# Kernel optimization log

Measured on AMD Instinct MI355X. Metric: run time of the kernel, lower is better.

## Reference

```python
import jax, jax.numpy as jnp
import numpy as np

DIM = 1024
HEADS = 16
DIM_HEAD = 64
NUM_KV_HEADS = 4
INNER = HEADS * DIM_HEAD          # 1024
KV_DIM = NUM_KV_HEADS * DIM_HEAD  # 256
SCALE = DIM_HEAD ** -0.5


def setup_inputs() -> dict:
    key = jax.random.key(0)
    ks = jax.random.split(key, 7)
    B, S = 2, 2048
    x = jax.random.normal(ks[0], (B, S, DIM), dtype=jnp.float32)
    init = lambda k, shape: jax.random.normal(k, shape, dtype=jnp.float32) * (shape[0] ** -0.5)
    return {
        "x": x,
        "ln_gamma": jnp.ones((DIM,), jnp.float32),
        "ln_beta": jnp.zeros((DIM,), jnp.float32),
        "w_q": init(ks[1], (DIM, INNER)),
        "w_k": init(ks[2], (DIM, KV_DIM)),
        "w_v": init(ks[3], (DIM, KV_DIM)),
        "w_o": init(ks[4], (INNER, DIM)),
        "b_o": jnp.zeros((DIM,), jnp.float32),
    }


def reference(x, ln_gamma, ln_beta, w_q, w_k, w_v, w_o, b_o):
    B, S, _ = x.shape
    g, hpg, d = NUM_KV_HEADS, HEADS // NUM_KV_HEADS, DIM_HEAD
    # LayerNorm (eps matches torch default 1e-5)
    mu = jnp.mean(x, axis=-1, keepdims=True)
    var = jnp.mean((x - mu) ** 2, axis=-1, keepdims=True)
    xn = (x - mu) * jax.lax.rsqrt(var + 1e-5) * ln_gamma + ln_beta
    # projections
    q = xn @ w_q  # [B,S,INNER]
    k = xn @ w_k  # [B,S,KV_DIM]
    v = xn @ w_v
    # q: b s (g hpg d) -> b g hpg s d  (head index h = g*hpg + i, g-major)
    q = q.reshape(B, S, g, hpg, d).transpose(0, 2, 3, 1, 4)
    k = k.reshape(B, S, g, d).transpose(0, 2, 1, 3)  # [B,g,S,d]
    v = v.reshape(B, S, g, d).transpose(0, 2, 1, 3)
    dots = jnp.einsum('bghqd,bgkd->bghqk', q, k) * SCALE
    attn = jax.nn.softmax(dots, axis=-1)
    out = jnp.einsum('bghqk,bgkd->bghqd', attn, v)
    # b g hpg s d -> b s (g hpg d)
    out = out.transpose(0, 3, 1, 2, 4).reshape(B, S, INNER)
    return out @ w_o + b_o
```

## Files before the change

kernel.cpp:

```cpp
#include <hip/hip_runtime.h>

typedef unsigned short u16;
typedef __bf16 bf16x8 __attribute__((ext_vector_type(8)));
typedef short s16x4 __attribute__((ext_vector_type(4)));
typedef float f32x4 __attribute__((ext_vector_type(4)));

__device__ __forceinline__ u16 f32_to_bf16(float f) {
  union { float f; unsigned u; } v; v.f = f;
  unsigned r = v.u + 0x7FFFu + ((v.u >> 16) & 1u);
  return (u16)(r >> 16);
}
__device__ __forceinline__ unsigned f2u(float f) { union { float f; unsigned u; } v; v.f = f; return v.u; }
__device__ __forceinline__ float u2f(unsigned u) { union { unsigned u; float f; } v; v.u = u; return v.f; }

__global__ __launch_bounds__(256) void transpose_cvt_multi(
    const float* __restrict__ w_q, const float* __restrict__ w_k,
    const float* __restrict__ w_v, const float* __restrict__ w_o,
    u16* __restrict__ wqkvT, u16* __restrict__ woT) {
  const float* src; u16* dst; int N;
  switch (blockIdx.z) {
    case 0: src = w_q; dst = wqkvT; N = 1024; break;
    case 1: src = w_k; dst = wqkvT + 1024 * 1024; N = 256; break;
    case 2: src = w_v; dst = wqkvT + 1280 * 1024; N = 256; break;
    default: src = w_o; dst = woT; N = 1024; break;
  }
  int n0 = blockIdx.x * 64;
  if (n0 >= N) return;
  const int K = 1024;
  __shared__ float tile[64][65];
  int k0 = blockIdx.y * 64;
  int t = threadIdx.x;
  int c = t & 63, r4 = t >> 6;
#pragma unroll
  for (int rr = r4; rr < 64; rr += 4)
    tile[rr][c] = src[(size_t)(k0 + rr) * N + n0 + c];
  __syncthreads();
#pragma unroll
  for (int rr = r4; rr < 64; rr += 4)
    dst[(size_t)(n0 + rr) * K + k0 + c] = f32_to_bf16(tile[c][rr]);
}

__global__ __launch_bounds__(256) void ln_kernel(
    const float* __restrict__ x, const float* __restrict__ gamma,
    const float* __restrict__ beta, u16* __restrict__ xn) {
  int row = blockIdx.x;
  int t = threadIdx.x;
  const float4 v = ((const float4*)(x + (size_t)row * 1024))[t];
  float s = v.x + v.y + v.z + v.w;
  float ss = v.x * v.x + v.y * v.y + v.z * v.z + v.w * v.w;
#pragma unroll
  for (int m = 1; m < 64; m <<= 1) {
    s += __shfl_xor(s, m, 64);
    ss += __shfl_xor(ss, m, 64);
  }
  __shared__ float as_[4], ass[4];
  int wave = t >> 6;
  if ((t & 63) == 0) { as_[wave] = s; ass[wave] = ss; }
  __syncthreads();
  s = as_[0] + as_[1] + as_[2] + as_[3];
  ss = ass[0] + ass[1] + ass[2] + ass[3];
  float mu = s * (1.0f / 1024.0f);
  float var = ss * (1.0f / 1024.0f) - mu * mu;
  float rstd = rsqrtf(var + 1e-5f);
  float4 g = ((const float4*)gamma)[t];
  float4 b = ((const float4*)beta)[t];
  uint2 o;
  o.x = (unsigned)f32_to_bf16((v.x - mu) * rstd * g.x + b.x) |
        ((unsigned)f32_to_bf16((v.y - mu) * rstd * g.y + b.y) << 16);
  o.y = (unsigned)f32_to_bf16((v.z - mu) * rstd * g.z + b.z) |
        ((unsigned)f32_to_bf16((v.w - mu) * rstd * g.w + b.w) << 16);
  ((uint2*)(xn + (size_t)row * 1024))[t] = o;
}

template <int OUT_MODE>
__global__ __launch_bounds__(256) void gemm_bf16_k(
    const u16* __restrict__ A, const u16* __restrict__ Bt,
    void* __restrict__ Cv, const float* __restrict__ bias,
    int M, int N, int K, int ldc) {
  __shared__ __align__(16) u16 sA[128 * 72];
  __shared__ __align__(16) u16 sB[128 * 72];
  int t = threadIdx.x;
  int m0 = blockIdx.y * 128, n0 = blockIdx.x * 128;
  int wave = t >> 6, lane = t & 63;
  int wm = wave >> 1, wn = wave & 1;
  int l15 = lane & 15, quad = lane >> 4;

  f32x4 acc[4][4];
#pragma unroll
  for (int i = 0; i < 4; i++)
#pragma unroll
    for (int j = 0; j < 4; j++) acc[i][j] = f32x4{0.f, 0.f, 0.f, 0.f};

  int r = t >> 3, q = t & 7;
  const u16* Ap = A + (size_t)(m0 + r) * K + q * 8;
  const u16* Bp = Bt + (size_t)(n0 + r) * K + q * 8;

  for (int k0 = 0; k0 < K; k0 += 64) {
    uint4 av0 = *(const uint4*)(Ap + k0);
    uint4 av1 = *(const uint4*)(Ap + k0 + (size_t)32 * K);
    uint4 av2 = *(const uint4*)(Ap + k0 + (size_t)64 * K);
    uint4 av3 = *(const uint4*)(Ap + k0 + (size_t)96 * K);
    uint4 bv0 = *(const uint4*)(Bp + k0);
    uint4 bv1 = *(const uint4*)(Bp + k0 + (size_t)32 * K);
    uint4 bv2 = *(const uint4*)(Bp + k0 + (size_t)64 * K);
    uint4 bv3 = *(const uint4*)(Bp + k0 + (size_t)96 * K);
    __syncthreads();
    *(uint4*)&sA[(r) * 72 + q * 8] = av0;
    *(uint4*)&sA[(r + 32) * 72 + q * 8] = av1;
    *(uint4*)&sA[(r + 64) * 72 + q * 8] = av2;
    *(uint4*)&sA[(r + 96) * 72 + q * 8] = av3;
    *(uint4*)&sB[(r) * 72 + q * 8] = bv0;
    *(uint4*)&sB[(r + 32) * 72 + q * 8] = bv1;
    *(uint4*)&sB[(r + 64) * 72 + q * 8] = bv2;
    *(uint4*)&sB[(r + 96) * 72 + q * 8] = bv3;
    __syncthreads();
#pragma unroll
    for (int ks = 0; ks < 2; ++ks) {
      bf16x8 af[4], bf[4];
#pragma unroll
      for (int mi = 0; mi < 4; mi++)
        af[mi] = *(const bf16x8*)&sA[(wm * 64 + mi * 16 + l15) * 72 + ks * 32 + quad * 8];
#pragma unroll
      for (int ni = 0; ni < 4; ni++)
        bf[ni] = *(const bf16x8*)&sB[(wn * 64 + ni * 16 + l15) * 72 + ks * 32 + quad * 8];
#pragma unroll
      for (int mi = 0; mi < 4; mi++)
#pragma unroll
        for (int ni = 0; ni < 4; ni++)
          acc[mi][ni] = __builtin_amdgcn_mfma_f32_16x16x32_bf16(
              af[mi], bf[ni], acc[mi][ni], 0, 0, 0);
    }
  }
#pragma unroll
  for (int mi = 0; mi < 4; mi++)
#pragma unroll
    for (int ni = 0; ni < 4; ni++) {
      int row = m0 + wm * 64 + mi * 16 + quad * 4;
      int col = n0 + wn * 64 + ni * 16 + l15;
#pragma unroll
      for (int rr = 0; rr < 4; rr++) {
        float vv = acc[mi][ni][rr];
        if (OUT_MODE == 0)
          ((u16*)Cv)[(size_t)(row + rr) * ldc + col] = f32_to_bf16(vv);
        else
          ((float*)Cv)[(size_t)(row + rr) * ldc + col] = vv + bias[col];
      }
    }
}

__global__ __launch_bounds__(256) void attn_kernel(
    const u16* __restrict__ qkv, u16* __restrict__ attn_out) {
  const int LD = 1536;
  int qt = blockIdx.x;
  int bh = blockIdx.y;
  int b = bh >> 4, h = bh & 15, g = h >> 2;

  __shared__ __align__(16) u16 sK[64 * 72];
  __shared__ __align__(16) u16 sV[64 * 72];

  int t = threadIdx.x, wave = t >> 6, lane = t & 63;
  int l15 = lane & 15, quad = lane >> 4;

  const u16* qbase = qkv + (size_t)(b * 2048 + qt * 64) * LD + h * 64;
  const u16* kbase = qkv + (size_t)(b * 2048) * LD + 1024 + g * 64;
  const u16* vbase = kbase + 256;

  bf16x8 qf[2];
#pragma unroll
  for (int ks = 0; ks < 2; ++ks)
    qf[ks] = *(const bf16x8*)(qbase + (size_t)(wave * 16 + l15) * LD + ks * 32 + quad * 8);

  f32x4 oacc[4];
#pragma unroll
  for (int i = 0; i < 4; i++) oacc[i] = f32x4{0.f, 0.f, 0.f, 0.f};
  float lsum = 0.f;

  const float cexp = 0.125f * 1.44269504088896f;
  int sr = t >> 3, sq = t & 7;
  int vkp = (t & 31) * 2, vdc = (t >> 5) * 8;

  uint4 ka0, ka1, va0, va1;
  {
    const u16* kp0 = kbase + (size_t)sr * LD + sq * 8;
    ka0 = *(const uint4*)kp0;
    ka1 = *(const uint4*)(kp0 + (size_t)32 * LD);
    const u16* vp0 = vbase + (size_t)vkp * LD + vdc;
    va0 = *(const uint4*)vp0;
    va1 = *(const uint4*)(vp0 + LD);
  }

  for (int kt = 0; kt < 32; ++kt) {
    __syncthreads();
    *(uint4*)&sK[sr * 72 + sq * 8] = ka0;
    *(uint4*)&sK[(sr + 32) * 72 + sq * 8] = ka1;
    {
      const unsigned* aw = (const unsigned*)&va0;
      const unsigned* bw = (const unsigned*)&va1;
#pragma unroll
      for (int w = 0; w < 4; ++w) {
        unsigned lo = (aw[w] & 0xFFFFu) | (bw[w] << 16);
        unsigned hi = (aw[w] >> 16) | (bw[w] & 0xFFFF0000u);
        *(unsigned*)&sV[(vdc + 2 * w) * 72 + vkp] = lo;
        *(unsigned*)&sV[(vdc + 2 * w + 1) * 72 + vkp] = hi;
      }
    }
    __syncthreads();

    if (kt < 31) {
      const u16* kp0 = kbase + (size_t)((kt + 1) * 64 + sr) * LD + sq * 8;
      ka0 = *(const uint4*)kp0;
      ka1 = *(const uint4*)(kp0 + (size_t)32 * LD);
      const u16* vp0 = vbase + (size_t)((kt + 1) * 64 + vkp) * LD + vdc;
      va0 = *(const uint4*)vp0;
      va1 = *(const uint4*)(vp0 + LD);
    }

    f32x4 sacc[4];
#pragma unroll
    for (int i = 0; i < 4; i++) sacc[i] = f32x4{0.f, 0.f, 0.f, 0.f};
#pragma unroll
    for (int ni = 0; ni < 4; ++ni)
#pragma unroll
      for (int ks = 0; ks < 2; ++ks) {
        bf16x8 kf = *(const bf16x8*)&sK[(ni * 16 + l15) * 72 + ks * 32 + quad * 8];
        sacc[ni] = __builtin_amdgcn_mfma_f32_16x16x32_bf16(kf, qf[ks], sacc[ni], 0, 0, 0);
      }

    s16x4 pf[4];
#pragma unroll
    for (int ni = 0; ni < 4; ++ni) {
      unsigned r0, r1, r2, r3;
      {
        float p = __builtin_amdgcn_exp2f(sacc[ni][0] * cexp);
        r0 = (f2u(p) + 0x8000u) & 0xFFFF0000u; lsum += u2f(r0);
        p = __builtin_amdgcn_exp2f(sacc[ni][1] * cexp);
        r1 = (f2u(p) + 0x8000u) & 0xFFFF0000u; lsum += u2f(r1);
        p = __builtin_amdgcn_exp2f(sacc[ni][2] * cexp);
        r2 = (f2u(p) + 0x8000u) & 0xFFFF0000u; lsum += u2f(r2);
        p = __builtin_amdgcn_exp2f(sacc[ni][3] * cexp);
        r3 = (f2u(p) + 0x8000u) & 0xFFFF0000u; lsum += u2f(r3);
      }
      uint2 pk;
      pk.x = (r0 >> 16) | r1;
      pk.y = (r2 >> 16) | r3;
      pf[ni] = *(s16x4*)&pk;
    }

#pragma unroll
    for (int md = 0; md < 4; ++md)
#pragma unroll
      for (int ni = 0; ni < 4; ++ni) {
        s16x4 vf = *(const s16x4*)&sV[(md * 16 + l15) * 72 + ni * 16 + quad * 4];
        oacc[md] = __builtin_amdgcn_mfma_f32_16x16x16bf16_1k(vf, pf[ni], oacc[md], 0, 0, 0);
      }
  }

  lsum += __shfl_xor(lsum, 16, 64);
  lsum += __shfl_xor(lsum, 32, 64);
  float rinv = 1.0f / lsum;

  u16* obase = attn_out + (size_t)(b * 2048 + qt * 64 + wave * 16 + l15) * 1024 +
               h * 64 + quad * 4;
#pragma unroll
  for (int md = 0; md < 4; ++md) {
    unsigned r0 = (f2u(oacc[md][0] * rinv) + 0x8000u) & 0xFFFF0000u;
    unsigned r1 = (f2u(oacc[md][1] * rinv) + 0x8000u) & 0xFFFF0000u;
    unsigned r2 = (f2u(oacc[md][2] * rinv) + 0x8000u) & 0xFFFF0000u;
    unsigned r3 = (f2u(oacc[md][3] * rinv) + 0x8000u) & 0xFFFF0000u;
    uint2 o;
    o.x = (r0 >> 16) | r1;
    o.y = (r2 >> 16) | r3;
    *(uint2*)(obase + md * 16) = o;
  }
}

extern "C" void kernel_launch(void* const* d_in, const int* in_sizes, int n_in,
                              void* d_out, int out_size, void* d_ws, size_t ws_size,
                              hipStream_t stream) {
  const float* x = (const float*)d_in[0];
  const float* gamma = (const float*)d_in[1];
  const float* beta = (const float*)d_in[2];
  const float* w_q = (const float*)d_in[3];
  const float* w_k = (const float*)d_in[4];
  const float* w_v = (const float*)d_in[5];
  const float* w_o = (const float*)d_in[6];
  const float* b_o = (const float*)d_in[7];
  float* out = (float*)d_out;

  char* ws = (char*)d_ws;
  u16* wqkvT = (u16*)ws;
  u16* woT = (u16*)(ws + 3u * 1024 * 1024);
  u16* xn = (u16*)(ws + 5u * 1024 * 1024);
  u16* qkv = (u16*)(ws + 13u * 1024 * 1024);
  u16* attn = (u16*)(ws + 25u * 1024 * 1024);

  transpose_cvt_multi<<<dim3(16, 16, 4), 256, 0, stream>>>(w_q, w_k, w_v, w_o,
                                                           wqkvT, woT);
  ln_kernel<<<4096, 256, 0, stream>>>(x, gamma, beta, xn);

  gemm_bf16_k<0><<<dim3(12, 32), 256, 0, stream>>>(xn, wqkvT, qkv, nullptr,
                                                   4096, 1536, 1024, 1536);

  attn_kernel<<<dim3(32, 32), 256, 0, stream>>>(qkv, attn);

  gemm_bf16_k<1><<<dim3(8, 32), 256, 0, stream>>>(attn, woT, out, b_o,
                                                  4096, 1024, 1024, 1024);
}
```

Before: 201.2 us.

## Enlarge attention query tile per wave, fold softmax scale into Q projection

Each wave now handles 64 query rows instead of 16, so every K/V tile staged in shared memory is reused across four query subtiles and the attention grid shrinks from 32x32 to 8x32 blocks. The softmax scale times log2(e) is applied in the QKV GEMM epilogue to the Q columns, which removes a multiply per score. The row-sum is now computed with an MFMA against a ones vector instead of scalar adds, and bf16 packing uses the hardware pack-convert builtin when it is available. In exchange, register pressure rises a lot (64 output accumulators plus the P fragments per wave), there are fewer blocks to fill the GPU, and Q is stored pre-scaled in bf16.

```diff
diff --git a/kernel.cpp b/kernel.cpp
--- a/kernel.cpp
+++ b/kernel.cpp
@@ -2,6 +2,7 @@
 
 typedef unsigned short u16;
 typedef __bf16 bf16x8 __attribute__((ext_vector_type(8)));
+typedef __bf16 bf16x2 __attribute__((ext_vector_type(2)));
 typedef short s16x4 __attribute__((ext_vector_type(4)));
 typedef float f32x4 __attribute__((ext_vector_type(4)));
 
@@ -11,7 +12,15 @@
   return (u16)(r >> 16);
 }
 __device__ __forceinline__ unsigned f2u(float f) { union { float f; unsigned u; } v; v.f = f; return v.u; }
-__device__ __forceinline__ float u2f(unsigned u) { union { unsigned u; float f; } v; v.u = u; return v.f; }
+
+__device__ __forceinline__ unsigned pack2bf16(float a, float b) {
+#if __has_builtin(__builtin_amdgcn_cvt_pk_bf16_f32)
+  bf16x2 r = __builtin_amdgcn_cvt_pk_bf16_f32(a, b);
+  return *(unsigned*)&r;
+#else
+  return (f2u(a) >> 16) | (f2u(b) & 0xFFFF0000u);
+#endif
+}
 
 __global__ __launch_bounds__(256) void transpose_cvt_multi(
     const float* __restrict__ w_q, const float* __restrict__ w_k,
@@ -65,10 +74,8 @@
   float4 g = ((const float4*)gamma)[t];
   float4 b = ((const float4*)beta)[t];
   uint2 o;
-  o.x = (unsigned)f32_to_bf16((v.x - mu) * rstd * g.x + b.x) |
-        ((unsigned)f32_to_bf16((v.y - mu) * rstd * g.y + b.y) << 16);
-  o.y = (unsigned)f32_to_bf16((v.z - mu) * rstd * g.z + b.z) |
-        ((unsigned)f32_to_bf16((v.w - mu) * rstd * g.w + b.w) << 16);
+  o.x = pack2bf16((v.x - mu) * rstd * g.x + b.x, (v.y - mu) * rstd * g.y + b.y);
+  o.y = pack2bf16((v.z - mu) * rstd * g.z + b.z, (v.w - mu) * rstd * g.w + b.w);
   ((uint2*)(xn + (size_t)row * 1024))[t] = o;
 }
 
@@ -76,7 +83,7 @@
 __global__ __launch_bounds__(256) void gemm_bf16_k(
     const u16* __restrict__ A, const u16* __restrict__ Bt,
     void* __restrict__ Cv, const float* __restrict__ bias,
-    int M, int N, int K, int ldc) {
+    int M, int N, int K, int ldc, float qscale, int qcols) {
   __shared__ __align__(16) u16 sA[128 * 72];
   __shared__ __align__(16) u16 sB[128 * 72];
   int t = threadIdx.x;
@@ -140,10 +147,12 @@
 #pragma unroll
       for (int rr = 0; rr < 4; rr++) {
         float vv = acc[mi][ni][rr];
-        if (OUT_MODE == 0)
-          ((u16*)Cv)[(size_t)(row + rr) * ldc + col] = f32_to_bf16(vv);
-        else
+        if (OUT_MODE == 0) {
+          float sc = (col < qcols) ? qscale : 1.0f;
+          ((u16*)Cv)[(size_t)(row + rr) * ldc + col] = f32_to_bf16(vv * sc);
+        } else {
           ((float*)Cv)[(size_t)(row + rr) * ldc + col] = vv + bias[col];
+        }
       }
     }
 }
@@ -161,21 +170,29 @@
   int t = threadIdx.x, wave = t >> 6, lane = t & 63;
   int l15 = lane & 15, quad = lane >> 4;
 
-  const u16* qbase = qkv + (size_t)(b * 2048 + qt * 64) * LD + h * 64;
+  const u16* qbase = qkv + (size_t)(b * 2048 + qt * 256 + wave * 64) * LD + h * 64;
   const u16* kbase = qkv + (size_t)(b * 2048) * LD + 1024 + g * 64;
   const u16* vbase = kbase + 256;
 
-  bf16x8 qf[2];
-#pragma unroll
-  for (int ks = 0; ks < 2; ++ks)
-    qf[ks] = *(const bf16x8*)(qbase + (size_t)(wave * 16 + l15) * LD + ks * 32 + quad * 8);
-
-  f32x4 oacc[4];
-#pragma unroll
-  for (int i = 0; i < 4; i++) oacc[i] = f32x4{0.f, 0.f, 0.f, 0.f};
-  float lsum = 0.f;
-
-  const float cexp = 0.125f * 1.44269504088896f;
+  bf16x8 qf[4][2];
+#pragma unroll
+  for (int qs = 0; qs < 4; ++qs)
+#pragma unroll
+    for (int ks = 0; ks < 2; ++ks)
+      qf[qs][ks] = *(const bf16x8*)(qbase + (size_t)(qs * 16 + l15) * LD + ks * 32 + quad * 8);
+
+  f32x4 oacc[4][4];
+  f32x4 lacc[4];
+#pragma unroll
+  for (int qs = 0; qs < 4; ++qs) {
+    lacc[qs] = f32x4{0.f, 0.f, 0.f, 0.f};
+#pragma unroll
+    for (int md = 0; md < 4; ++md) oacc[qs][md] = f32x4{0.f, 0.f, 0.f, 0.f};
+  }
+
+  const s16x4 ones = {(short)0x3F80, (short)0x3F80, (short)0x3F80, (short)0x3F80};
+  const f32x4 fzero = {0.f, 0.f, 0.f, 0.f};
+
   int sr = t >> 3, sq = t & 7;
   int vkp = (t & 31) * 2, vdc = (t >> 5) * 8;
 
@@ -215,35 +232,30 @@
       va1 = *(const uint4*)(vp0 + LD);
     }
 
-    f32x4 sacc[4];
-#pragma unroll
-    for (int i = 0; i < 4; i++) sacc[i] = f32x4{0.f, 0.f, 0.f, 0.f};
-#pragma unroll
-    for (int ni = 0; ni < 4; ++ni)
-#pragma unroll
-      for (int ks = 0; ks < 2; ++ks) {
-        bf16x8 kf = *(const bf16x8*)&sK[(ni * 16 + l15) * 72 + ks * 32 + quad * 8];
-        sacc[ni] = __builtin_amdgcn_mfma_f32_16x16x32_bf16(kf, qf[ks], sacc[ni], 0, 0, 0);
+    s16x4 pf[4][4];
+#pragma unroll
+    for (int ni = 0; ni < 4; ++ni) {
+      bf16x8 kf0 = *(const bf16x8*)&sK[(ni * 16 + l15) * 72 + quad * 8];
+      bf16x8 kf1 = *(const bf16x8*)&sK[(ni * 16 + l15) * 72 + 32 + quad * 8];
+      f32x4 sacc[4];
+#pragma unroll
+      for (int qs = 0; qs < 4; ++qs)
+        sacc[qs] = __builtin_amdgcn_mfma_f32_16x16x32_bf16(kf0, qf[qs][0], fzero, 0, 0, 0);
+#pragma unroll
+      for (int qs = 0; qs < 4; ++qs)
+        sacc[qs] = __builtin_amdgcn_mfma_f32_16x16x32_bf16(kf1, qf[qs][1], sacc[qs], 0, 0, 0);
+#pragma unroll
+      for (int qs = 0; qs < 4; ++qs) {
+        float p0 = __builtin_amdgcn_exp2f(sacc[qs][0]);
+        float p1 = __builtin_amdgcn_exp2f(sacc[qs][1]);
+        float p2 = __builtin_amdgcn_exp2f(sacc[qs][2]);
+        float p3 = __builtin_amdgcn_exp2f(sacc[qs][3]);
+        uint2 pk;
+        pk.x = pack2bf16(p0, p1);
+        pk.y = pack2bf16(p2, p3);
+        pf[qs][ni] = *(s16x4*)&pk;
+        lacc[qs] = __builtin_amdgcn_mfma_f32_16x16x16bf16_1k(ones, pf[qs][ni], lacc[qs], 0, 0, 0);
       }
-
-    s16x4 pf[4];
-#pragma unroll
-    for (int ni = 0; ni < 4; ++ni) {
-      unsigned r0, r1, r2, r3;
-      {
-        float p = __builtin_amdgcn_exp2f(sacc[ni][0] * cexp);
-        r0 = (f2u(p) + 0x8000u) & 0xFFFF0000u; lsum += u2f(r0);
-        p = __builtin_amdgcn_exp2f(sacc[ni][1] * cexp);
-        r1 = (f2u(p) + 0x8000u) & 0xFFFF0000u; lsum += u2f(r1);
-        p = __builtin_amdgcn_exp2f(sacc[ni][2] * cexp);
-        r2 = (f2u(p) + 0x8000u) & 0xFFFF0000u; lsum += u2f(r2);
-        p = __builtin_amdgcn_exp2f(sacc[ni][3] * cexp);
-        r3 = (f2u(p) + 0x8000u) & 0xFFFF0000u; lsum += u2f(r3);
-      }
-      uint2 pk;
-      pk.x = (r0 >> 16) | r1;
-      pk.y = (r2 >> 16) | r3;
-      pf[ni] = *(s16x4*)&pk;
     }
 
 #pragma unroll
@@ -251,26 +263,25 @@
 #pragma unroll
       for (int ni = 0; ni < 4; ++ni) {
         s16x4 vf = *(const s16x4*)&sV[(md * 16 + l15) * 72 + ni * 16 + quad * 4];
-        oacc[md] = __builtin_amdgcn_mfma_f32_16x16x16bf16_1k(vf, pf[ni], oacc[md], 0, 0, 0);
+#pragma unroll
+        for (int qs = 0; qs < 4; ++qs)
+          oacc[qs][md] = __builtin_amdgcn_mfma_f32_16x16x16bf16_1k(vf, pf[qs][ni], oacc[qs][md], 0, 0, 0);
       }
   }
 
-  lsum += __shfl_xor(lsum, 16, 64);
-  lsum += __shfl_xor(lsum, 32, 64);
-  float rinv = 1.0f / lsum;
-
-  u16* obase = attn_out + (size_t)(b * 2048 + qt * 64 + wave * 16 + l15) * 1024 +
-               h * 64 + quad * 4;
-#pragma unroll
-  for (int md = 0; md < 4; ++md) {
-    unsigned r0 = (f2u(oacc[md][0] * rinv) + 0x8000u) & 0xFFFF0000u;
-    unsigned r1 = (f2u(oacc[md][1] * rinv) + 0x8000u) & 0xFFFF0000u;
-    unsigned r2 = (f2u(oacc[md][2] * rinv) + 0x8000u) & 0xFFFF0000u;
-    unsigned r3 = (f2u(oacc[md][3] * rinv) + 0x8000u) & 0xFFFF0000u;
-    uint2 o;
-    o.x = (r0 >> 16) | r1;
-    o.y = (r2 >> 16) | r3;
-    *(uint2*)(obase + md * 16) = o;
+#pragma unroll
+  for (int qs = 0; qs < 4; ++qs) {
+    float rinv = 1.0f / lacc[qs][0];
+    u16* obase = attn_out +
+                 (size_t)(b * 2048 + qt * 256 + wave * 64 + qs * 16 + l15) * 1024 +
+                 h * 64 + quad * 4;
+#pragma unroll
+    for (int md = 0; md < 4; ++md) {
+      uint2 o;
+      o.x = pack2bf16(oacc[qs][md][0] * rinv, oacc[qs][md][1] * rinv);
+      o.y = pack2bf16(oacc[qs][md][2] * rinv, oacc[qs][md][3] * rinv);
+      *(uint2*)(obase + md * 16) = o;
+    }
   }
 }
 
@@ -294,15 +305,19 @@
   u16* qkv = (u16*)(ws + 13u * 1024 * 1024);
   u16* attn = (u16*)(ws + 25u * 1024 * 1024);
 
+  const float cexp = 0.125f * 1.44269504088896f;
+
   transpose_cvt_multi<<<dim3(16, 16, 4), 256, 0, stream>>>(w_q, w_k, w_v, w_o,
                                                            wqkvT, woT);
   ln_kernel<<<4096, 256, 0, stream>>>(x, gamma, beta, xn);
 
   gemm_bf16_k<0><<<dim3(12, 32), 256, 0, stream>>>(xn, wqkvT, qkv, nullptr,
-                                                   4096, 1536, 1024, 1536);
-
-  attn_kernel<<<dim3(32, 32), 256, 0, stream>>>(qkv, attn);
+                                                   4096, 1536, 1024, 1536,
+                                                   cexp, 1024);
+
+  attn_kernel<<<dim3(8, 32), 256, 0, stream>>>(qkv, attn);
 
   gemm_bf16_k<1><<<dim3(8, 32), 256, 0, stream>>>(attn, woT, out, b_o,
-                                                  4096, 1024, 1024, 1024);
-}
+                                                  4096, 1024, 1024, 1024,
+                                                  1.0f, 0);
+}
```

Result: slower. 206.9 us (+2.9%).
